# Performance work log

Hardware: AMD Instinct MI355X
Metric: run time of the kernel (lower is better)

## Reference

```python
import jax, jax.numpy as jnp
import numpy as np

B, H, S, D = 4, 16, 2048, 64
ROPE_BASE = 10000.0


def _rope(x):
    # Rotate-half RoPE over the last dim, positions along the second-to-last dim.
    d = x.shape[-1]
    s = x.shape[-2]
    inv_freq = 1.0 / (ROPE_BASE ** (jnp.arange(0, d, 2, dtype=jnp.float32) / d))  # [D/2]
    ang = jnp.arange(s, dtype=jnp.float32)[:, None] * inv_freq                    # [S, D/2]
    cos, sin = jnp.cos(ang), jnp.sin(ang)
    x1, x2 = x[..., : d // 2], x[..., d // 2:]
    return jnp.concatenate([x1 * cos - x2 * sin, x1 * sin + x2 * cos], axis=-1).astype(x.dtype)


def setup_inputs() -> dict:
    key = jax.random.key(0)
    kq, kk, kv = jax.random.split(key, 3)
    q = jax.random.normal(kq, (B, H, S, D), dtype=jnp.float32)
    k = jax.random.normal(kk, (B, H, S, D), dtype=jnp.float32)
    v = jax.random.normal(kv, (B, H, S, D), dtype=jnp.float32)
    mask = jnp.tril(jnp.ones((S, S), dtype=bool))  # causal, broadcasts over [B,H,S,S]
    return {"q": q, "k": k, "v": v, "mask": mask}


def reference(q, k, v, mask):
    d_k = q.shape[-1]
    qr = _rope(q)
    kr = _rope(k)
    scores = jnp.einsum('bhqd,bhkd->bhqk', qr, kr) / jnp.sqrt(jnp.asarray(d_k, jnp.float32))
    scores = jnp.where(mask, scores, -jnp.inf)  # masked_fill(mask == False, -inf)
    probs = jax.nn.softmax(scores, axis=-1)
    return jnp.einsum('bhqk,bhkd->bhqd', probs, v)
```

## Files before the change

### kernel.cpp

```cpp
#include <hip/hip_runtime.h>
#include <hip/hip_bf16.h>
#include <math.h>

#define SS 2048
#define DD 64
#define BH 64
#define QT 64
#define KT 64
#define NT 256
#define NKT (SS / KT)
#define LQ 72
#define LOG2E 1.4426950408889634f
#define IFS (13.287712379549449f / 32.0f)

typedef __attribute__((ext_vector_type(8))) short s8v;
typedef __attribute__((ext_vector_type(4))) short s4v;
typedef __attribute__((ext_vector_type(4))) float f4v;

__device__ __forceinline__ short f2b(float x) {
  __hip_bfloat16 h = __float2bfloat16(x);
  return *reinterpret_cast<short*>(&h);
}

__device__ __forceinline__ void gload16(const void* g, void* l) {
  __builtin_amdgcn_global_load_lds(
      (const __attribute__((address_space(1))) void*)g,
      (__attribute__((address_space(3))) void*)l, 16, 0, 0);
}

template <int CTRL>
__device__ __forceinline__ float dppf(float x) {
  int i = __builtin_bit_cast(int, x);
  i = __builtin_amdgcn_update_dpp(i, i, CTRL, 0xf, 0xf, false);
  return __builtin_bit_cast(float, i);
}
__device__ __forceinline__ float rowmax16(float x) {
  x = fmaxf(x, dppf<0xB1>(x));
  x = fmaxf(x, dppf<0x4E>(x));
  x = fmaxf(x, dppf<0x124>(x));
  x = fmaxf(x, dppf<0x128>(x));
  return x;
}
__device__ __forceinline__ float rowsum16(float x) {
  x += dppf<0xB1>(x);
  x += dppf<0x4E>(x);
  x += dppf<0x124>(x);
  x += dppf<0x128>(x);
  return x;
}

__device__ __forceinline__ void rope_cs(int pos, int j, float& c, float& s) {
  float inv = exp2f(-(float)j * IFS);
  float ang = (float)pos * inv;
  __sincosf(ang, &s, &c);
}

__global__ __launch_bounds__(NT) void prep_kv_kernel(
    const float* __restrict__ kg, const float* __restrict__ vg,
    short* __restrict__ kr, short* __restrict__ vt) {
  __shared__ float Vs[KT][DD + 1];
  const int b = blockIdx.x;
  const int kt = b & 31;
  const int t = threadIdx.x;
  const size_t ofs = (size_t)b * (KT * DD);
  const float* ktile = kg + ofs;
  short* krt = kr + ofs;

#pragma unroll
  for (int i = 0; i < 8; ++i) {
    int idx = t + i * NT;
    int r = idx >> 5, j = idx & 31;
    float s, c;
    rope_cs(kt * KT + r, j, c, s);
    float x1 = ktile[r * DD + j], x2 = ktile[r * DD + j + 32];
    krt[r * DD + j] = f2b(x1 * c - x2 * s);
    krt[r * DD + j + 32] = f2b(x1 * s + x2 * c);
  }

  const float* vtile = vg + ofs;
#pragma unroll
  for (int i = 0; i < 4; ++i) {
    int s4 = t + i * NT;
    int r = s4 >> 4, c4 = (s4 & 15) * 4;
    float4 v = *(const float4*)&vtile[r * DD + c4];
    Vs[r][c4 + 0] = v.x;
    Vs[r][c4 + 1] = v.y;
    Vs[r][c4 + 2] = v.z;
    Vs[r][c4 + 3] = v.w;
  }
  __syncthreads();
  short* otile = vt + ofs;
#pragma unroll
  for (int i = 0; i < 2; ++i) {
    int c = t + i * NT;
    int d = c >> 3, k8 = (c & 7) * 8;
    s8v o;
#pragma unroll
    for (int u = 0; u < 8; ++u) {
      int kp = k8 + u;
      int src = ((kp & 3) << 4) + (kp >> 2);
      o[u] = f2b(Vs[src][d]);
    }
    *(s8v*)&otile[d * KT + k8] = o;
  }
}

__global__ __launch_bounds__(NT, 4) void attn_fast(
    const float* __restrict__ qg, const short* __restrict__ kr,
    const short* __restrict__ vt, float* __restrict__ og) {
  __shared__ __align__(16) short Ks[2][KT * DD];
  __shared__ __align__(16) short Vts[2][DD * KT];
  __shared__ __align__(16) short QP[QT * DD];

  const int tid = threadIdx.x;
  const int lane = tid & 63;
  const int wv = tid >> 6;
  const int quad = lane >> 4;
  const int lx = lane & 15;
  const int xb = lx & 7;
  const int foff0 = ((quad ^ xb) << 3);
  const int foff1 = (((quad | 4) ^ xb) << 3);

  const int bid = blockIdx.x;
  const int qt = NKT - 1 - (bid >> 6);
  const int bh = bid & 63;
  const int qbase = qt * QT;
  const float* Q = qg + (size_t)bh * SS * DD;
  float* O = og + (size_t)bh * SS * DD;
  const short* krh = kr + (size_t)bh * SS * DD;
  const short* vth = vt + (size_t)bh * SS * DD;

  int goff[2], loff[2];
#pragma unroll
  for (int i = 0; i < 2; ++i) {
    int c = wv * 128 + i * 64 + lane;
    int r = c >> 3, qp = c & 7;
    int qs = qp ^ (r & 7);
    goff[i] = r * DD + qs * 8;
    loff[i] = (wv * 128 + i * 64) * 8;
  }

#pragma unroll
  for (int i = 0; i < 2; ++i) {
    gload16(krh + goff[i], &Ks[0][loff[i]]);
    gload16(vth + goff[i], &Vts[0][loff[i]]);
  }

  const float qscale = 0.125f * LOG2E;
#pragma unroll
  for (int t = 0; t < 8; ++t) {
    int idx = tid + t * NT;
    int r = idx >> 5, j = idx & 31;
    float s, c;
    rope_cs(qbase + r, j, c, s);
    float x1 = Q[(size_t)(qbase + r) * DD + j];
    float x2 = Q[(size_t)(qbase + r) * DD + j + 32];
    int rb = r & 7;
    QP[r * DD + ((((j >> 3) ^ rb) << 3) | (j & 7))] = f2b((x1 * c - x2 * s) * qscale);
    QP[r * DD + (((((j >> 3) | 4) ^ rb) << 3) | (j & 7))] = f2b((x1 * s + x2 * c) * qscale);
  }
  __syncthreads();

  const int rq = wv * 16 + lx;
  s8v qf0 = *(const s8v*)&QP[rq * DD + foff0];
  s8v qf1 = *(const s8v*)&QP[rq * DD + foff1];

  const short bone = f2b(1.0f);
  s8v ones;
#pragma unroll
  for (int u = 0; u < 8; ++u) ones[u] = bone;

  short* Ps = &QP[wv * 16 * DD];

  f4v o_[4];
  f4v ol = (f4v){0.f, 0.f, 0.f, 0.f};
#pragma unroll
  for (int db = 0; db < 4; ++db) o_[db] = (f4v){0.f, 0.f, 0.f, 0.f};

  for (int kt = 0; kt <= qt; ++kt) {
    const int cur = kt & 1;
    if (kt) __syncthreads();

    if (kt < qt) {
      const short* ktile = krh + (size_t)(kt + 1) * (KT * DD);
      const short* vtile = vth + (size_t)(kt + 1) * (DD * KT);
      const int nxt = cur ^ 1;
#pragma unroll
      for (int i = 0; i < 2; ++i) {
        gload16(ktile + goff[i], &Ks[nxt][loff[i]]);
        gload16(vtile + goff[i], &Vts[nxt][loff[i]]);
      }
    }

    f4v sc[4];
#pragma unroll
    for (int nb = 0; nb < 4; ++nb) {
      const int rk = nb * 16 + lx;
      s8v kf0 = *(const s8v*)&Ks[cur][rk * DD + foff0];
      s8v kf1 = *(const s8v*)&Ks[cur][rk * DD + foff1];
      f4v z = (f4v){0.f, 0.f, 0.f, 0.f};
      z = __builtin_amdgcn_mfma_f32_16x16x32_bf16(qf0, kf0, z, 0, 0, 0);
      z = __builtin_amdgcn_mfma_f32_16x16x32_bf16(qf1, kf1, z, 0, 0, 0);
      sc[nb] = z;
    }

    if (kt == qt) {
#pragma unroll
      for (int nb = 0; nb < 4; ++nb)
#pragma unroll
        for (int r = 0; r < 4; ++r)
          if (nb * 16 + lx > wv * 16 + quad * 4 + r) sc[nb][r] = -INFINITY;
    }

#pragma unroll
    for (int r = 0; r < 4; ++r) {
      const int rl = quad * 4 + r;
      float p0 = __builtin_amdgcn_exp2f(sc[0][r]);
      float p1 = __builtin_amdgcn_exp2f(sc[1][r]);
      float p2 = __builtin_amdgcn_exp2f(sc[2][r]);
      float p3 = __builtin_amdgcn_exp2f(sc[3][r]);
      s4v pk = {f2b(p0), f2b(p1), f2b(p2), f2b(p3)};
      *(s4v*)&Ps[rl * DD + (((lx >> 1) ^ (rl & 7)) << 3) + ((lx & 1) << 2)] = pk;
    }

    s8v pf0 = *(const s8v*)&Ps[lx * DD + foff0];
    s8v pf1 = *(const s8v*)&Ps[lx * DD + foff1];
    ol = __builtin_amdgcn_mfma_f32_16x16x32_bf16(pf0, ones, ol, 0, 0, 0);
    ol = __builtin_amdgcn_mfma_f32_16x16x32_bf16(pf1, ones, ol, 0, 0, 0);
#pragma unroll
    for (int db = 0; db < 4; ++db) {
      const int rv = db * 16 + lx;
      s8v vf0 = *(const s8v*)&Vts[cur][rv * KT + foff0];
      s8v vf1 = *(const s8v*)&Vts[cur][rv * KT + foff1];
      o_[db] = __builtin_amdgcn_mfma_f32_16x16x32_bf16(pf0, vf0, o_[db], 0, 0, 0);
      o_[db] = __builtin_amdgcn_mfma_f32_16x16x32_bf16(pf1, vf1, o_[db], 0, 0, 0);
    }
  }

#pragma unroll
  for (int r = 0; r < 4; ++r) {
    float rinv = 1.0f / ol[r];
    int row = qbase + wv * 16 + quad * 4 + r;
#pragma unroll
    for (int db = 0; db < 4; ++db)
      O[(size_t)row * DD + db * 16 + lx] = o_[db][r] * rinv;
  }
}

__global__ __launch_bounds__(NT, 4) void attn_fallback(
    const float* __restrict__ qg, const float* __restrict__ kg,
    const float* __restrict__ vg, float* __restrict__ og) {
  __shared__ __align__(16) short Qs[64 * LQ];
  __shared__ __align__(16) short Ksh[64 * LQ];
  __shared__ __align__(16) short Vt[DD * LQ];
  __shared__ __align__(16) short Ps[4][16 * LQ];

  const int tid = threadIdx.x;
  const int lane = tid & 63;
  const int wv = tid >> 6;
  const int quad = lane >> 4;
  const int lx = lane & 15;

  const int bid = blockIdx.x;
  const int qt = NKT - 1 - (bid >> 6);
  const int bh = bid & 63;
  const int qbase = qt * 64;
  const size_t base = (size_t)bh * SS * DD;
  const float* Q = qg + base;
  const float* K = kg + base;
  const float* V = vg + base;
  float* O = og + base;

  const float qscale = 0.125f * LOG2E;
  for (int t = 0; t < 8; ++t) {
    int idx = tid + t * NT;
    int r = idx >> 5, j = idx & 31;
    float c, s;
    rope_cs(qbase + r, j, c, s);
    float x1 = Q[(size_t)(qbase + r) * DD + j];
    float x2 = Q[(size_t)(qbase + r) * DD + j + 32];
    Qs[r * LQ + j] = f2b((x1 * c - x2 * s) * qscale);
    Qs[r * LQ + j + 32] = f2b((x1 * s + x2 * c) * qscale);
  }
  __syncthreads();

  s8v qf0 = *(const s8v*)&Qs[(wv * 16 + lx) * LQ + quad * 8];
  s8v qf1 = *(const s8v*)&Qs[(wv * 16 + lx) * LQ + 32 + quad * 8];

  float m_[4], l_[4];
  f4v o_[4];
#pragma unroll
  for (int r = 0; r < 4; ++r) { m_[r] = -INFINITY; l_[r] = 0.f; }
#pragma unroll
  for (int db = 0; db < 4; ++db) o_[db] = (f4v){0.f, 0.f, 0.f, 0.f};

  for (int kt = 0; kt <= qt; ++kt) {
    const int kbase = kt * 64;
    __syncthreads();
    for (int t = 0; t < 8; ++t) {
      int idx = tid + t * NT;
      int r = idx >> 5, j = idx & 31;
      float c, s;
      rope_cs(kbase + r, j, c, s);
      float x1 = K[(size_t)(kbase + r) * DD + j];
      float x2 = K[(size_t)(kbase + r) * DD + j + 32];
      Ksh[r * LQ + j] = f2b(x1 * c - x2 * s);
      Ksh[r * LQ + j + 32] = f2b(x1 * s + x2 * c);
    }
    for (int t = 0; t < 4; ++t) {
      int i4 = tid + t * NT;
      int r = i4 >> 4, c4 = (i4 & 15) * 4;
      const float4 v = *(const float4*)&V[(size_t)(kbase + r) * DD + c4];
      Vt[(c4 + 0) * LQ + r] = f2b(v.x);
      Vt[(c4 + 1) * LQ + r] = f2b(v.y);
      Vt[(c4 + 2) * LQ + r] = f2b(v.z);
      Vt[(c4 + 3) * LQ + r] = f2b(v.w);
    }
    __syncthreads();

    f4v sc[4];
#pragma unroll
    for (int nb = 0; nb < 4; ++nb) {
      s8v kf0 = *(const s8v*)&Ksh[(nb * 16 + lx) * LQ + quad * 8];
      s8v kf1 = *(const s8v*)&Ksh[(nb * 16 + lx) * LQ + 32 + quad * 8];
      f4v z = (f4v){0.f, 0.f, 0.f, 0.f};
      z = __builtin_amdgcn_mfma_f32_16x16x32_bf16(qf0, kf0, z, 0, 0, 0);
      z = __builtin_amdgcn_mfma_f32_16x16x32_bf16(qf1, kf1, z, 0, 0, 0);
      sc[nb] = z;
    }
    if (kt == qt) {
#pragma unroll
      for (int nb = 0; nb < 4; ++nb)
#pragma unroll
        for (int r = 0; r < 4; ++r)
          if (kbase + nb * 16 + lx > qbase + wv * 16 + quad * 4 + r)
            sc[nb][r] = -INFINITY;
    }
#pragma unroll
    for (int r = 0; r < 4; ++r) {
      float mx = fmaxf(fmaxf(sc[0][r], sc[1][r]), fmaxf(sc[2][r], sc[3][r]));
      mx = rowmax16(mx);
      float mn = fmaxf(m_[r], mx);
      float al = __builtin_amdgcn_exp2f(m_[r] - mn);
      m_[r] = mn;
      float rs = 0.f;
#pragma unroll
      for (int nb = 0; nb < 4; ++nb) {
        float p = __builtin_amdgcn_exp2f(sc[nb][r] - mn);
        rs += p;
        Ps[wv][(quad * 4 + r) * LQ + nb * 16 + lx] = f2b(p);
      }
      rs = rowsum16(rs);
      l_[r] = l_[r] * al + rs;
      o_[0][r] *= al; o_[1][r] *= al; o_[2][r] *= al; o_[3][r] *= al;
    }
    s8v pf0 = *(const s8v*)&Ps[wv][lx * LQ + quad * 8];
    s8v pf1 = *(const s8v*)&Ps[wv][lx * LQ + 32 + quad * 8];
#pragma unroll
    for (int db = 0; db < 4; ++db) {
      s8v vf0 = *(const s8v*)&Vt[(db * 16 + lx) * LQ + quad * 8];
      s8v vf1 = *(const s8v*)&Vt[(db * 16 + lx) * LQ + 32 + quad * 8];
      o_[db] = __builtin_amdgcn_mfma_f32_16x16x32_bf16(pf0, vf0, o_[db], 0, 0, 0);
      o_[db] = __builtin_amdgcn_mfma_f32_16x16x32_bf16(pf1, vf1, o_[db], 0, 0, 0);
    }
  }
#pragma unroll
  for (int r = 0; r < 4; ++r) {
    float rinv = 1.0f / l_[r];
    int row = qbase + wv * 16 + quad * 4 + r;
#pragma unroll
    for (int db = 0; db < 4; ++db)
      O[(size_t)row * DD + db * 16 + lx] = o_[db][r] * rinv;
  }
}

extern "C" void kernel_launch(void* const* d_in, const int* in_sizes, int n_in,
                              void* d_out, int out_size, void* d_ws, size_t ws_size,
                              hipStream_t stream) {
  const float* q = (const float*)d_in[0];
  const float* k = (const float*)d_in[1];
  const float* v = (const float*)d_in[2];
  float* out = (float*)d_out;

  const size_t kr_bytes = (size_t)BH * SS * DD * sizeof(short);
  const size_t vt_bytes = kr_bytes;
  const size_t need = kr_bytes + vt_bytes;

  if (ws_size >= need) {
    short* kr = (short*)d_ws;
    short* vt = (short*)((char*)d_ws + kr_bytes);
    prep_kv_kernel<<<BH * NKT, NT, 0, stream>>>(k, v, kr, vt);
    attn_fast<<<dim3(BH * NKT), dim3(NT), 0, stream>>>(q, kr, vt, out);
  } else {
    attn_fallback<<<dim3(BH * NKT), dim3(NT), 0, stream>>>(q, k, v, out);
  }
}
```

Before: 196.4 us.

## Double query tile to 128 rows with 512-thread blocks sharing K/V tiles

Each block now handles 128 query rows with 8 waves instead of 64 rows with 4 waves, so every K/V tile staged in LDS is reused by twice as many waves. Each thread issues one async global-to-LDS load per tile instead of two. The causal mask is applied to the last two key tiles using absolute positions. This halves K/V traffic per query but produces fewer, larger blocks, and because waves 0-3 have nothing to compute on the final tile, causal load balance gets coarser.

```diff
diff --git a/kernel.cpp b/kernel.cpp
--- a/kernel.cpp
+++ b/kernel.cpp
@@ -5,10 +5,12 @@
 #define SS 2048
 #define DD 64
 #define BH 64
-#define QT 64
 #define KT 64
 #define NT 256
 #define NKT (SS / KT)
+#define QTT 128
+#define NTA 512
+#define NQT (SS / QTT)
 #define LQ 72
 #define LOG2E 1.4426950408889634f
 #define IFS (13.287712379549449f / 32.0f)
@@ -105,12 +107,12 @@
   }
 }
 
-__global__ __launch_bounds__(NT, 4) void attn_fast(
+__global__ __launch_bounds__(NTA, 6) void attn_fast(
     const float* __restrict__ qg, const short* __restrict__ kr,
     const short* __restrict__ vt, float* __restrict__ og) {
   __shared__ __align__(16) short Ks[2][KT * DD];
   __shared__ __align__(16) short Vts[2][DD * KT];
-  __shared__ __align__(16) short QP[QT * DD];
+  __shared__ __align__(16) short QP[QTT * DD];
 
   const int tid = threadIdx.x;
   const int lane = tid & 63;
@@ -122,34 +124,27 @@
   const int foff1 = (((quad | 4) ^ xb) << 3);
 
   const int bid = blockIdx.x;
-  const int qt = NKT - 1 - (bid >> 6);
+  const int qb = (NQT - 1) - (bid >> 6);
   const int bh = bid & 63;
-  const int qbase = qt * QT;
+  const int qbase = qb * QTT;
+  const int ktmax = 2 * qb + 1;
   const float* Q = qg + (size_t)bh * SS * DD;
   float* O = og + (size_t)bh * SS * DD;
   const short* krh = kr + (size_t)bh * SS * DD;
   const short* vth = vt + (size_t)bh * SS * DD;
 
-  int goff[2], loff[2];
-#pragma unroll
-  for (int i = 0; i < 2; ++i) {
-    int c = wv * 128 + i * 64 + lane;
-    int r = c >> 3, qp = c & 7;
-    int qs = qp ^ (r & 7);
-    goff[i] = r * DD + qs * 8;
-    loff[i] = (wv * 128 + i * 64) * 8;
-  }
-
-#pragma unroll
-  for (int i = 0; i < 2; ++i) {
-    gload16(krh + goff[i], &Ks[0][loff[i]]);
-    gload16(vth + goff[i], &Vts[0][loff[i]]);
-  }
+  const int r_dma = tid >> 3;
+  const int qs_dma = (tid & 7) ^ (r_dma & 7);
+  const int goff = r_dma * DD + qs_dma * 8;
+  const int loff = wv * 512;
+
+  gload16(krh + goff, &Ks[0][loff]);
+  gload16(vth + goff, &Vts[0][loff]);
 
   const float qscale = 0.125f * LOG2E;
 #pragma unroll
   for (int t = 0; t < 8; ++t) {
-    int idx = tid + t * NT;
+    int idx = tid + t * NTA;
     int r = idx >> 5, j = idx & 31;
     float s, c;
     rope_cs(qbase + r, j, c, s);
@@ -177,19 +172,16 @@
 #pragma unroll
   for (int db = 0; db < 4; ++db) o_[db] = (f4v){0.f, 0.f, 0.f, 0.f};
 
-  for (int kt = 0; kt <= qt; ++kt) {
+  for (int kt = 0; kt <= ktmax; ++kt) {
     const int cur = kt & 1;
     if (kt) __syncthreads();
 
-    if (kt < qt) {
+    if (kt < ktmax) {
       const short* ktile = krh + (size_t)(kt + 1) * (KT * DD);
       const short* vtile = vth + (size_t)(kt + 1) * (DD * KT);
       const int nxt = cur ^ 1;
-#pragma unroll
-      for (int i = 0; i < 2; ++i) {
-        gload16(ktile + goff[i], &Ks[nxt][loff[i]]);
-        gload16(vtile + goff[i], &Vts[nxt][loff[i]]);
-      }
+      gload16(ktile + goff, &Ks[nxt][loff]);
+      gload16(vtile + goff, &Vts[nxt][loff]);
     }
 
     f4v sc[4];
@@ -204,12 +196,13 @@
       sc[nb] = z;
     }
 
-    if (kt == qt) {
+    if (kt >= ktmax - 1) {
+      const int kb = kt * KT;
 #pragma unroll
       for (int nb = 0; nb < 4; ++nb)
 #pragma unroll
         for (int r = 0; r < 4; ++r)
-          if (nb * 16 + lx > wv * 16 + quad * 4 + r) sc[nb][r] = -INFINITY;
+          if (kb + nb * 16 + lx > qbase + wv * 16 + quad * 4 + r) sc[nb][r] = -INFINITY;
     }
 
 #pragma unroll
@@ -390,7 +383,7 @@
     short* kr = (short*)d_ws;
     short* vt = (short*)((char*)d_ws + kr_bytes);
     prep_kv_kernel<<<BH * NKT, NT, 0, stream>>>(k, v, kr, vt);
-    attn_fast<<<dim3(BH * NKT), dim3(NT), 0, stream>>>(q, kr, vt, out);
+    attn_fast<<<dim3(BH * NQT), dim3(NTA), 0, stream>>>(q, kr, vt, out);
   } else {
     attn_fallback<<<dim3(BH * NKT), dim3(NT), 0, stream>>>(q, k, v, out);
   }
```

New measurement: 192.4 us. 2.0% less time.
